# Optimization experiments

Hardware: AMD Instinct MI355X
Metric: run time of the kernel (lower is better)

The kernel has to match this reference:

```python
import jax, jax.numpy as jnp
import numpy as np

B, IN_CAPS, IN_DIM = 64, 2048, 16
NUM_CAPS, OUT_DIM = 32, 16
NUM_ROUTING = 3


def squash(v, axis=-1):
    # scale = |v|^2 / (1 + |v|^2) / |v|  (faithful to source, no epsilon)
    s2 = jnp.sum(jnp.square(v), axis=axis, keepdims=True)
    scale = s2 / (1.0 + s2) / jnp.sqrt(s2)
    return scale * v


def setup_inputs() -> dict:
    key = jax.random.key(0)
    k1, k2 = jax.random.split(key)
    inputs = jax.random.normal(k1, (B, IN_CAPS, IN_DIM), dtype=jnp.float32)
    # glorot-ish scaled transform matrices
    W = jax.random.normal(k2, (IN_CAPS, NUM_CAPS, IN_DIM, OUT_DIM), dtype=jnp.float32) * 0.05
    return {"inputs": inputs, "W": W}


def reference(inputs, W):
    # Prediction vectors u_hat[b,i,k,:] = inputs[b,i,:] @ W[i,k,:,:]
    u_hat = jnp.einsum('bid,ikdo->biko', inputs, W)  # [B, I, K, O]
    # Routing logits b (per-batch; source initializes from zeros and accumulates agreement)
    b = jnp.zeros(u_hat.shape[:3], dtype=u_hat.dtype)  # [B, I, K]
    v = None
    for i in range(NUM_ROUTING):
        c = jax.nn.softmax(b, axis=2)                      # coupling coeffs over output caps K
        s = jnp.einsum('bik,biko->bko', c, u_hat)          # weighted sum over input caps I
        v = squash(s)                                      # [B, K, O]
        if i != NUM_ROUTING - 1:
            b = b + jnp.einsum('biko,bko->bik', u_hat, v)  # agreement update
    return v  # [B, NUM_CAPS, OUT_DIM]
```

## Files before the change

### kernel.cpp

```cpp
#include <hip/hip_runtime.h>
#include <math.h>
#include <stdint.h>

#define NB 64
#define NI 2048
#define NK 32
#define ND 16

typedef _Float16 h2t   __attribute__((ext_vector_type(2)));
typedef _Float16 f16x4 __attribute__((ext_vector_type(4)));
typedef float    f32x4 __attribute__((ext_vector_type(4)));

#if defined(__has_builtin)
#if __has_builtin(__builtin_amdgcn_global_load_lds)
#define HAVE_GLL 1
#endif
#endif
#ifndef HAVE_GLL
#define HAVE_GLL 0
#endif

static __device__ __forceinline__ uint32_t pack_h2(float a, float b) {
    h2t p; p.x = (_Float16)a; p.y = (_Float16)b;
    return __builtin_bit_cast(uint32_t, p);
}

static __device__ __forceinline__ float swz_xor16(float x) {
    int v = __builtin_amdgcn_ds_swizzle(__builtin_bit_cast(int, x), 0x401F);
    return __builtin_bit_cast(float, v);
}
static __device__ __forceinline__ float xreduce_o(float p) {
    p += swz_xor16(p);
    p += __shfl_xor(p, 32);
    return p;
}

__global__ __launch_bounds__(256)
void conv_wx(const float* __restrict__ Wg, uint32_t* __restrict__ Wh,
             const float* __restrict__ X,  uint32_t* __restrict__ XT)
{
    __shared__ float tile[32 * 264];
    const int t = threadIdx.x;
    if (blockIdx.x < 2048) {
        const int i = blockIdx.x;
        const float4* src = (const float4*)(Wg + (size_t)i * 8192);
#pragma unroll
        for (int j = 0; j < 8; ++j) {
            const int f4 = t + j * 256;
            const int k  = f4 >> 6;
            const int r4 = f4 & 63;
            *(float4*)(&tile[k * 264 + r4 * 4]) = src[f4];
        }
        __syncthreads();
        const int T  = t >> 3;
        const int l0 = (t & 7) * 8;
        const float* s = tile + T * 264;
        uint2* dst = (uint2*)(Wh + (size_t)i * 4096) + T * 64 + l0;
#pragma unroll
        for (int n = 0; n < 8; ++n) {
            const int l = l0 + n;
            const int q = l >> 4, r = l & 15;
            uint2 u;
            u.x = pack_h2(s[(4 * q + 0) * 16 + r], s[(4 * q + 1) * 16 + r]);
            u.y = pack_h2(s[(4 * q + 2) * 16 + r], s[(4 * q + 3) * 16 + r]);
            dst[n] = u;
        }
    } else {
        const int g = (blockIdx.x - 2048) * 256 + t;
        const int b = g >> 11, i = g & 2047;
        const float4* src = (const float4*)(X + ((size_t)b * 2048 + i) * 16);
        const float4 f0 = src[0], f1 = src[1], f2 = src[2], f3 = src[3];
        uint4 o0, o1;
        o0.x = pack_h2(f0.x, f0.y); o0.y = pack_h2(f0.z, f0.w);
        o0.z = pack_h2(f1.x, f1.y); o0.w = pack_h2(f1.z, f1.w);
        o1.x = pack_h2(f2.x, f2.y); o1.y = pack_h2(f2.z, f2.w);
        o1.z = pack_h2(f3.x, f3.y); o1.w = pack_h2(f3.z, f3.w);
        uint4* dst = (uint4*)(XT + (size_t)i * 512 + b * 8);
        dst[0] = o0; dst[1] = o1;
    }
}

template<int VMODE>
__global__ __launch_bounds__(256, 3)
void caps_pass_m(const uint32_t* __restrict__ XT,
                 const uint32_t* __restrict__ Wh,
                 const float* __restrict__ V,
                 uint32_t* __restrict__ part_h)
{
    constexpr int IC = 16;
    __shared__ uint32_t Ws[2][4096];
    __shared__ uint32_t Xs[2048];
    __shared__ float    Ep[2][4][16];

    const int t = threadIdx.x;
    const int l = t & 63;
    const int w = t >> 6;
    const int r = l & 15;
    const int q = l >> 4;

    const int wg     = blockIdx.x;
    const int xcd    = wg & 7;
    const int slot   = wg >> 3;
    const int ichunk = xcd * 16 + (slot >> 2);
    const int bg     = slot & 3;
    const int i0 = ichunk * IC;
    const int b0 = bg * 16;

    f32x4 s_acc[8];
#pragma unroll
    for (int tt = 0; tt < 8; ++tt) s_acc[tt] = (f32x4){0.f, 0.f, 0.f, 0.f};

    f32x4 v_r[8];
    if constexpr (VMODE == 1) {
#pragma unroll
        for (int tt = 0; tt < 8; ++tt)
            v_r[tt] = *(const f32x4*)(V + ((size_t)(b0 + r) * NK + (8 * w + tt)) * 16 + 4 * q);
    }

    {
        const int ig = t >> 4, uu = t & 15;
        const uint4* src = (const uint4*)(XT + (size_t)(i0 + ig) * 512 + b0 * 8);
        *(uint4*)&Xs[ig * 128 + uu * 4]        = src[uu];
        *(uint4*)&Xs[ig * 128 + (uu + 16) * 4] = src[uu + 16];
    }

#if HAVE_GLL
#define STAGE_T(sl, tile)                                                      \
    {                                                                          \
        const size_t ibase_ = (size_t)(tile) * 4096;                           \
        _Pragma("unroll")                                                      \
        for (int jj = 0; jj < 4; ++jj) {                                       \
            const int p = w * 4 + jj;                                          \
            __builtin_amdgcn_global_load_lds(                                  \
                (const __attribute__((address_space(1))) void*)(Wh + ibase_ + p * 256 + l * 4), \
                (__attribute__((address_space(3))) void*)&Ws[sl][p * 256], 16, 0, 0); \
        }                                                                      \
    }
#define WAIT_V(n) { asm volatile("s_waitcnt vmcnt(" #n ")" ::: "memory");      \
                    __builtin_amdgcn_sched_barrier(0); }
#else
#define STAGE_T(sl, tile)                                                      \
    {                                                                          \
        const size_t ibase_ = (size_t)(tile) * 4096;                           \
        _Pragma("unroll")                                                      \
        for (int jj = 0; jj < 4; ++jj) {                                       \
            const int p = w * 4 + jj;                                          \
            ((uint4*)&Ws[sl][p * 256])[l] = *(const uint4*)(Wh + ibase_ + p * 256 + l * 4); \
        }                                                                      \
    }
#define WAIT_V(n) { asm volatile("s_waitcnt vmcnt(0) lgkmcnt(0)" ::: "memory");\
                    __builtin_amdgcn_sched_barrier(0); }
#endif
#define BAR_E() asm volatile("s_waitcnt lgkmcnt(0)\ns_barrier" ::: "memory");
#define STAGE_GUARD() { asm volatile("s_waitcnt lgkmcnt(0)" ::: "memory");     \
                        __builtin_amdgcn_sched_barrier(0); }

    __syncthreads();

    STAGE_T(0, i0)
    STAGE_T(1, i0 + 1)

    for (int ii = 0; ii < IC; ++ii) {
        const int cur = ii & 1;
        if (ii + 1 < IC) { WAIT_V(4) } else { WAIT_V(0) }

        const f16x4 xb = *(const f16x4*)&Xs[ii * 128 + r * 8 + q * 2];

        if constexpr (VMODE == 0) {
#pragma unroll
            for (int tt = 0; tt < 8; ++tt) {
                const f16x4 a = *(const f16x4*)&Ws[cur][(w * 8 + tt) * 128 + l * 2];
                s_acc[tt] = __builtin_amdgcn_mfma_f32_16x16x16f16(a, xb, s_acc[tt], 0, 0, 0);
            }
        } else {
            f32x4 um[8];
#pragma unroll
            for (int tt = 0; tt < 8; ++tt) {
                const f16x4 a = *(const f16x4*)&Ws[cur][(w * 8 + tt) * 128 + l * 2];
                um[tt] = __builtin_amdgcn_mfma_f32_16x16x16f16(
                    a, xb, (f32x4){0.f, 0.f, 0.f, 0.f}, 0, 0, 0);
            }
            float e[8];
            float esp = 0.f;
#pragma unroll
            for (int tt = 0; tt < 8; ++tt) {
                float p = um[tt][0] * v_r[tt][0];
                p = fmaf(um[tt][1], v_r[tt][1], p);
                p = fmaf(um[tt][2], v_r[tt][2], p);
                p = fmaf(um[tt][3], v_r[tt][3], p);
                p = xreduce_o(p);
                e[tt] = __expf(p);
                esp += e[tt];
            }
            if (q == 0) Ep[ii & 1][w][r] = esp;
            BAR_E();
            const float es = Ep[ii & 1][0][r] + Ep[ii & 1][1][r]
                           + Ep[ii & 1][2][r] + Ep[ii & 1][3][r];
            const float ci = __builtin_amdgcn_rcpf(es);
#pragma unroll
            for (int tt = 0; tt < 8; ++tt) {
                const float c = e[tt] * ci;
                s_acc[tt][0] = fmaf(c, um[tt][0], s_acc[tt][0]);
                s_acc[tt][1] = fmaf(c, um[tt][1], s_acc[tt][1]);
                s_acc[tt][2] = fmaf(c, um[tt][2], s_acc[tt][2]);
                s_acc[tt][3] = fmaf(c, um[tt][3], s_acc[tt][3]);
            }
        }

        if (ii + 2 < IC) {
            STAGE_GUARD();
            STAGE_T(cur, i0 + ii + 2)
        }
    }
#undef STAGE_T
#undef WAIT_V
#undef BAR_E
#undef STAGE_GUARD

    uint32_t* base = part_h + (size_t)(bg * 128 + ichunk) * 4096 + r * 256 + 2 * q;
#pragma unroll
    for (int tt = 0; tt < 8; ++tt) {
        uint2 st;
        st.x = pack_h2(s_acc[tt][0], s_acc[tt][1]);
        st.y = pack_h2(s_acc[tt][2], s_acc[tt][3]);
        *(uint2*)(base + (8 * w + tt) * 8) = st;
    }
}

template<int RMODE>
__global__ __launch_bounds__(256)
void caps_reduce(const uint32_t* __restrict__ part_h,
                 const float* __restrict__ S0red,
                 float* __restrict__ S0out,
                 float* __restrict__ Vout)
{
    __shared__ float2 red[4][64];
    const int t   = threadIdx.x;
    const int jl  = t & 63;
    const int qc  = t >> 6;
    const int jb  = blockIdx.x * 64;
    const int j   = jb + jl;
    const int b   = j >> 8;
    const int bg  = b >> 4;
    const int loc = (b & 15) * 256 + (j & 255);
    const uint32_t* p = part_h + ((size_t)(bg * 128 + qc * 32)) * 4096 + loc;
    float sx = 0.f, sy = 0.f;
#pragma unroll 8
    for (int ic = 0; ic < 32; ++ic) {
        h2t v = __builtin_bit_cast(h2t, p[(size_t)ic * 4096]);
        sx += (float)v.x; sy += (float)v.y;
    }
    red[qc][jl] = make_float2(sx, sy);
    __syncthreads();
    if (t < 64) {
        const int jj = jb + t;
        float2 a0 = red[0][t], a1 = red[1][t], a2 = red[2][t], a3 = red[3][t];
        const float tx = a0.x + a1.x + a2.x + a3.x;
        const float ty = a0.y + a1.y + a2.y + a3.y;
        if constexpr (RMODE == 0) {
            S0out[2 * jj]     = tx;
            S0out[2 * jj + 1] = ty;
            const float vx = tx * (1.0f / 32.0f), vy = ty * (1.0f / 32.0f);
            float sq = vx * vx + vy * vy;
#pragma unroll
            for (int mask = 4; mask >= 1; mask >>= 1) sq += __shfl_xor(sq, mask);
            const float sc = sqrtf(sq) / (1.0f + sq);
            Vout[2 * jj]     = vx * sc;
            Vout[2 * jj + 1] = vy * sc;
        } else if constexpr (RMODE == 1) {
            const float v0x = S0red[2 * jj] * (1.0f / 32.0f);
            const float v0y = S0red[2 * jj + 1] * (1.0f / 32.0f);
            float sq0 = v0x * v0x + v0y * v0y;
#pragma unroll
            for (int mask = 4; mask >= 1; mask >>= 1) sq0 += __shfl_xor(sq0, mask);
            const float sc0 = sqrtf(sq0) / (1.0f + sq0);
            float sq1 = tx * tx + ty * ty;
#pragma unroll
            for (int mask = 4; mask >= 1; mask >>= 1) sq1 += __shfl_xor(sq1, mask);
            const float sc1 = sqrtf(sq1) / (1.0f + sq1);
            Vout[2 * jj]     = fmaf(v0x, sc0, tx * sc1);
            Vout[2 * jj + 1] = fmaf(v0y, sc0, ty * sc1);
        } else {
            float sq = tx * tx + ty * ty;
#pragma unroll
            for (int mask = 4; mask >= 1; mask >>= 1) sq += __shfl_xor(sq, mask);
            const float sc = sqrtf(sq) / (1.0f + sq);
            Vout[2 * jj]     = tx * sc;
            Vout[2 * jj + 1] = ty * sc;
        }
    }
}

template<int VMODE>
__global__ __launch_bounds__(256, 4)
void caps_pass_f32(const float* __restrict__ X,
                   const float* __restrict__ Wg,
                   const float* __restrict__ S0,
                   const float* __restrict__ S1,
                   float* __restrict__ Sout)
{
    constexpr int IC = 8;
    __shared__ float Ws[8192];
    __shared__ float Xs[2048];

    const int t   = threadIdx.x;
    const int kk  = t & 31;
    const int oh  = (t >> 5) & 1;
    const int bq4 = t >> 6;

    const int wg     = blockIdx.x;
    const int xcd    = wg & 7;
    const int slot   = wg >> 3;
    const int ichunk = xcd * 32 + (slot >> 2);
    const int bg     = slot & 3;
    const int i0 = ichunk * IC;
    const int b0 = bg * 16;

    float s_acc[4][8];
#pragma unroll
    for (int bb = 0; bb < 4; ++bb)
#pragma unroll
        for (int o = 0; o < 8; ++o) s_acc[bb][o] = 0.f;

    float v_r[4][8];
    if constexpr (VMODE >= 1) {
#pragma unroll
        for (int bb = 0; bb < 4; ++bb) {
            const int b = b0 + bq4 * 4 + bb;
            const float* p0 = S0 + ((size_t)b * NK + kk) * 16 + oh * 8;
            float4 a = *(const float4*)(p0);
            float4 c = *(const float4*)(p0 + 4);
            float val0[8] = {a.x,a.y,a.z,a.w,c.x,c.y,c.z,c.w};
            float sq0 = 0.f;
#pragma unroll
            for (int o = 0; o < 8; ++o) { val0[o] *= (1.0f/32.0f); sq0 = fmaf(val0[o], val0[o], sq0); }
            sq0 += __shfl_xor(sq0, 32);
            const float sc0 = sqrtf(sq0) / (1.0f + sq0);
#pragma unroll
            for (int o = 0; o < 8; ++o) v_r[bb][o] = val0[o] * sc0;
            if constexpr (VMODE == 2) {
                const float* p1 = S1 + ((size_t)b * NK + kk) * 16 + oh * 8;
                float4 a1 = *(const float4*)(p1);
                float4 c1 = *(const float4*)(p1 + 4);
                float val1[8] = {a1.x,a1.y,a1.z,a1.w,c1.x,c1.y,c1.z,c1.w};
                float sq1 = 0.f;
#pragma unroll
                for (int o = 0; o < 8; ++o) sq1 = fmaf(val1[o], val1[o], sq1);
                sq1 += __shfl_xor(sq1, 32);
                const float sc1 = sqrtf(sq1) / (1.0f + sq1);
#pragma unroll
                for (int o = 0; o < 8; ++o) v_r[bb][o] = fmaf(val1[o], sc1, v_r[bb][o]);
            }
        }
    }

    {
        const int xb   = t >> 4;
        const int xig  = t & 7;
        const int half = (t >> 3) & 1;
        const float* xp = X + (size_t)(b0 + xb) * (NI * ND) + (size_t)(i0 + xig) * ND + half * 8;
        float4 f0 = *(const float4*)(xp);
        float4 f1 = *(const float4*)(xp + 4);
        float vals[8] = {f0.x,f0.y,f0.z,f0.w,f1.x,f1.y,f1.z,f1.w};
        const int m = (xig & 7) << 3;
#pragma unroll
        for (int jj = 0; jj < 8; ++jj) {
            const int d = half * 8 + jj;
            Xs[xig * 256 + ((16 * d + xb) ^ m)] = vals[jj];
        }
    }

    for (int ii = 0; ii < IC; ++ii) {
        const int i = i0 + ii;
        __syncthreads();
        {
            const float4* wsrc = (const float4*)(Wg + (size_t)i * 8192);
#pragma unroll
            for (int j = 0; j < 8; ++j) {
                float4 val = wsrc[t + j * 256];
                const int k = (t >> 6) + 4 * j;
                ((float4*)Ws)[k * 64 + ((t & 63) ^ (k & 7))] = val;
            }
        }
        __syncthreads();

        const int xm = (ii & 7) << 3;
        float u[4][8];
        if constexpr (VMODE >= 1) {
#pragma unroll
            for (int bb = 0; bb < 4; ++bb)
#pragma unroll
                for (int o = 0; o < 8; ++o) u[bb][o] = 0.f;
        }
#pragma unroll
        for (int d = 0; d < 16; ++d) {
            const float4 x4 = *(const float4*)(&Xs[ii * 256 + ((16 * d + 4 * bq4) ^ xm)]);
            float wvv[8];
            {
                const float4 wA = ((const float4*)Ws)[kk * 64 + ((d * 4 + oh * 2)     ^ (kk & 7))];
                const float4 wB = ((const float4*)Ws)[kk * 64 + ((d * 4 + oh * 2 + 1) ^ (kk & 7))];
                wvv[0]=wA.x; wvv[1]=wA.y; wvv[2]=wA.z; wvv[3]=wA.w;
                wvv[4]=wB.x; wvv[5]=wB.y; wvv[6]=wB.z; wvv[7]=wB.w;
            }
            if constexpr (VMODE >= 1) {
#pragma unroll
                for (int o = 0; o < 8; ++o) {
                    u[0][o] = fmaf(x4.x, wvv[o], u[0][o]);
                    u[1][o] = fmaf(x4.y, wvv[o], u[1][o]);
                    u[2][o] = fmaf(x4.z, wvv[o], u[2][o]);
                    u[3][o] = fmaf(x4.w, wvv[o], u[3][o]);
                }
            } else {
#pragma unroll
                for (int o = 0; o < 8; ++o) {
                    s_acc[0][o] = fmaf(x4.x, wvv[o], s_acc[0][o]);
                    s_acc[1][o] = fmaf(x4.y, wvv[o], s_acc[1][o]);
                    s_acc[2][o] = fmaf(x4.z, wvv[o], s_acc[2][o]);
                    s_acc[3][o] = fmaf(x4.w, wvv[o], s_acc[3][o]);
                }
            }
        }

        if constexpr (VMODE >= 1) {
#pragma unroll
            for (int bb = 0; bb < 4; ++bb) {
                float lg = 0.f;
#pragma unroll
                for (int o = 0; o < 8; ++o) lg = fmaf(u[bb][o], v_r[bb][o], lg);
                lg += __shfl_xor(lg, 32);
                float m = lg;
#pragma unroll
                for (int mask = 16; mask >= 1; mask >>= 1)
                    m = fmaxf(m, __shfl_xor(m, mask));
                const float e = __expf(lg - m);
                float ssum = e;
#pragma unroll
                for (int mask = 16; mask >= 1; mask >>= 1)
                    ssum += __shfl_xor(ssum, mask);
                const float c = e / ssum;
#pragma unroll
                for (int o = 0; o < 8; ++o)
                    s_acc[bb][o] = fmaf(c, u[bb][o], s_acc[bb][o]);
            }
        }
    }

#pragma unroll
    for (int bb = 0; bb < 4; ++bb) {
        float* sp = Sout + ((size_t)(b0 + bq4 * 4 + bb) * NK + kk) * 16 + oh * 8;
#pragma unroll
        for (int o = 0; o < 8; ++o) atomicAdd(sp + o, s_acc[bb][o]);
    }
}

__global__ __launch_bounds__(256)
void squash_kernel(const float* __restrict__ S, float* __restrict__ Vout)
{
    const int idx = blockIdx.x * 256 + threadIdx.x;
    float val = S[idx];
    float sq = val * val;
#pragma unroll
    for (int mask = 8; mask >= 1; mask >>= 1) sq += __shfl_xor(sq, mask);
    const float sc = sqrtf(sq) / (1.0f + sq);
    Vout[idx] = val * sc;
}

extern "C" void kernel_launch(void* const* d_in, const int* in_sizes, int n_in,
                              void* d_out, int out_size, void* d_ws, size_t ws_size,
                              hipStream_t stream)
{
    const float* X  = (const float*)d_in[0];
    const float* Wg = (const float*)d_in[1];
    float* out = (float*)d_out;

    const size_t WHU   = (size_t)2048 * 4096;
    const size_t XHU   = (size_t)64 * 2048 * 8;
    const size_t PARTU = (size_t)512 * 4096;
    const size_t need  = (WHU + XHU + PARTU) * 4 + 3 * 32768 * 4;

    const dim3 blk(256), pgrid(512), rgrid(256);

    if (ws_size >= need) {
        uint32_t* Wh   = (uint32_t*)d_ws;
        uint32_t* XT   = Wh + WHU;
        uint32_t* part = XT + XHU;
        float* s0      = (float*)(part + PARTU);
        float* v0      = s0 + 32768;
        float* v01     = v0 + 32768;

        conv_wx<<<dim3(2560), blk, 0, stream>>>(Wg, Wh, X, XT);

        caps_pass_m<0><<<pgrid, blk, 0, stream>>>(XT, Wh, nullptr, part);
        caps_reduce<0><<<rgrid, blk, 0, stream>>>(part, nullptr, s0, v0);
        caps_pass_m<1><<<pgrid, blk, 0, stream>>>(XT, Wh, v0, part);
        caps_reduce<1><<<rgrid, blk, 0, stream>>>(part, s0, nullptr, v01);
        caps_pass_m<1><<<pgrid, blk, 0, stream>>>(XT, Wh, v01, part);
        caps_reduce<2><<<rgrid, blk, 0, stream>>>(part, nullptr, nullptr, out);
    } else {
        float* s0 = (float*)d_ws;
        float* s1 = s0 + 32768;
        float* s2 = s1 + 32768;
        hipMemsetAsync(d_ws, 0, (size_t)3 * 32768 * sizeof(float), stream);
        caps_pass_f32<0><<<dim3(1024), blk, 0, stream>>>(X, Wg, nullptr, nullptr, s0);
        caps_pass_f32<1><<<dim3(1024), blk, 0, stream>>>(X, Wg, s0, nullptr, s1);
        caps_pass_f32<2><<<dim3(1024), blk, 0, stream>>>(X, Wg, s0, s1, s2);
        squash_kernel<<<dim3(128), blk, 0, stream>>>(s2, out);
    }
}
```

Before: 95.68 us.

## Widen capsule pass blocks to 32 batches with 512 threads to reuse W tiles

Each caps_pass_m block now covers 32 batch rows instead of 16 and uses 8 waves of 512 threads, with each wave doing 4 output capsules for two batch halves. Each staged W tile is reused across twice as many batches, so W traffic from global memory and the grid size are both halved. The partial-sum layout and the reduce kernel indexing are updated to match. In exchange there are fewer blocks (256) to fill the GPU, larger LDS per block, a softmax barrier per half, and a new launch bound of 512 threads that changes register limits.

Result: slower. 117.7 us (+23.0%).

```diff
diff --git a/kernel.cpp b/kernel.cpp
--- a/kernel.cpp
+++ b/kernel.cpp
@@ -81,7 +81,7 @@
 }
 
 template<int VMODE>
-__global__ __launch_bounds__(256, 3)
+__global__ __launch_bounds__(512, 4)
 void caps_pass_m(const uint32_t* __restrict__ XT,
                  const uint32_t* __restrict__ Wh,
                  const float* __restrict__ V,
@@ -89,8 +89,8 @@
 {
     constexpr int IC = 16;
     __shared__ uint32_t Ws[2][4096];
-    __shared__ uint32_t Xs[2048];
-    __shared__ float    Ep[2][4][16];
+    __shared__ uint32_t Xs[4096];
+    __shared__ float    Ep[2][2][8][16];
 
     const int t = threadIdx.x;
     const int l = t & 63;
@@ -101,52 +101,52 @@
     const int wg     = blockIdx.x;
     const int xcd    = wg & 7;
     const int slot   = wg >> 3;
-    const int ichunk = xcd * 16 + (slot >> 2);
-    const int bg     = slot & 3;
+    const int ichunk = xcd * 16 + (slot >> 1);
+    const int bg     = slot & 1;
     const int i0 = ichunk * IC;
-    const int b0 = bg * 16;
-
-    f32x4 s_acc[8];
-#pragma unroll
-    for (int tt = 0; tt < 8; ++tt) s_acc[tt] = (f32x4){0.f, 0.f, 0.f, 0.f};
-
-    f32x4 v_r[8];
+    const int b0 = bg * 32;
+
+    f32x4 s_acc[2][4];
+#pragma unroll
+    for (int h = 0; h < 2; ++h)
+#pragma unroll
+        for (int tt = 0; tt < 4; ++tt) s_acc[h][tt] = (f32x4){0.f, 0.f, 0.f, 0.f};
+
+    f32x4 v_r[2][4];
     if constexpr (VMODE == 1) {
 #pragma unroll
-        for (int tt = 0; tt < 8; ++tt)
-            v_r[tt] = *(const f32x4*)(V + ((size_t)(b0 + r) * NK + (8 * w + tt)) * 16 + 4 * q);
+        for (int h = 0; h < 2; ++h)
+#pragma unroll
+            for (int tt = 0; tt < 4; ++tt)
+                v_r[h][tt] = *(const f32x4*)(V + ((size_t)(b0 + h * 16 + r) * NK + (4 * w + tt)) * 16 + 4 * q);
     }
 
     {
-        const int ig = t >> 4, uu = t & 15;
-        const uint4* src = (const uint4*)(XT + (size_t)(i0 + ig) * 512 + b0 * 8);
-        *(uint4*)&Xs[ig * 128 + uu * 4]        = src[uu];
-        *(uint4*)&Xs[ig * 128 + (uu + 16) * 4] = src[uu + 16];
+        const int ig = t >> 5, b32 = t & 31;
+        const uint4* src = (const uint4*)(XT + (size_t)(i0 + ig) * 512 + b0 * 8 + b32 * 8);
+        *(uint4*)&Xs[ig * 256 + b32 * 8]     = src[0];
+        *(uint4*)&Xs[ig * 256 + b32 * 8 + 4] = src[1];
     }
 
 #if HAVE_GLL
 #define STAGE_T(sl, tile)                                                      \
     {                                                                          \
-        const size_t ibase_ = (size_t)(tile) * 4096;                           \
-        _Pragma("unroll")                                                      \
-        for (int jj = 0; jj < 4; ++jj) {                                       \
-            const int p = w * 4 + jj;                                          \
-            __builtin_amdgcn_global_load_lds(                                  \
-                (const __attribute__((address_space(1))) void*)(Wh + ibase_ + p * 256 + l * 4), \
-                (__attribute__((address_space(3))) void*)&Ws[sl][p * 256], 16, 0, 0); \
-        }                                                                      \
+        const size_t ibase_ = (size_t)(tile) * 4096 + w * 512;                 \
+        __builtin_amdgcn_global_load_lds(                                      \
+            (const __attribute__((address_space(1))) void*)(Wh + ibase_ + l * 4), \
+            (__attribute__((address_space(3))) void*)&Ws[sl][w * 512], 16, 0, 0); \
+        __builtin_amdgcn_global_load_lds(                                      \
+            (const __attribute__((address_space(1))) void*)(Wh + ibase_ + 256 + l * 4), \
+            (__attribute__((address_space(3))) void*)&Ws[sl][w * 512 + 256], 16, 0, 0); \
     }
 #define WAIT_V(n) { asm volatile("s_waitcnt vmcnt(" #n ")" ::: "memory");      \
                     __builtin_amdgcn_sched_barrier(0); }
 #else
 #define STAGE_T(sl, tile)                                                      \
     {                                                                          \
-        const size_t ibase_ = (size_t)(tile) * 4096;                           \
-        _Pragma("unroll")                                                      \
-        for (int jj = 0; jj < 4; ++jj) {                                       \
-            const int p = w * 4 + jj;                                          \
-            ((uint4*)&Ws[sl][p * 256])[l] = *(const uint4*)(Wh + ibase_ + p * 256 + l * 4); \
-        }                                                                      \
+        const size_t ibase_ = (size_t)(tile) * 4096 + w * 512;                 \
+        ((uint4*)&Ws[sl][w * 512])[l]       = *(const uint4*)(Wh + ibase_ + l * 4); \
+        ((uint4*)&Ws[sl][w * 512 + 256])[l] = *(const uint4*)(Wh + ibase_ + 256 + l * 4); \
     }
 #define WAIT_V(n) { asm volatile("s_waitcnt vmcnt(0) lgkmcnt(0)" ::: "memory");\
                     __builtin_amdgcn_sched_barrier(0); }
@@ -162,48 +162,55 @@
 
     for (int ii = 0; ii < IC; ++ii) {
         const int cur = ii & 1;
-        if (ii + 1 < IC) { WAIT_V(4) } else { WAIT_V(0) }
-
-        const f16x4 xb = *(const f16x4*)&Xs[ii * 128 + r * 8 + q * 2];
+        if (ii + 1 < IC) { WAIT_V(2) } else { WAIT_V(0) }
+
+        const f16x4 xb0 = *(const f16x4*)&Xs[ii * 256 + (0 * 16 + r) * 8 + q * 2];
+        const f16x4 xb1 = *(const f16x4*)&Xs[ii * 256 + (1 * 16 + r) * 8 + q * 2];
 
         if constexpr (VMODE == 0) {
 #pragma unroll
-            for (int tt = 0; tt < 8; ++tt) {
-                const f16x4 a = *(const f16x4*)&Ws[cur][(w * 8 + tt) * 128 + l * 2];
-                s_acc[tt] = __builtin_amdgcn_mfma_f32_16x16x16f16(a, xb, s_acc[tt], 0, 0, 0);
+            for (int tt = 0; tt < 4; ++tt) {
+                const f16x4 a = *(const f16x4*)&Ws[cur][(4 * w + tt) * 128 + l * 2];
+                s_acc[0][tt] = __builtin_amdgcn_mfma_f32_16x16x16f16(a, xb0, s_acc[0][tt], 0, 0, 0);
+                s_acc[1][tt] = __builtin_amdgcn_mfma_f32_16x16x16f16(a, xb1, s_acc[1][tt], 0, 0, 0);
             }
         } else {
-            f32x4 um[8];
-#pragma unroll
-            for (int tt = 0; tt < 8; ++tt) {
-                const f16x4 a = *(const f16x4*)&Ws[cur][(w * 8 + tt) * 128 + l * 2];
-                um[tt] = __builtin_amdgcn_mfma_f32_16x16x16f16(
-                    a, xb, (f32x4){0.f, 0.f, 0.f, 0.f}, 0, 0, 0);
-            }
-            float e[8];
-            float esp = 0.f;
-#pragma unroll
-            for (int tt = 0; tt < 8; ++tt) {
-                float p = um[tt][0] * v_r[tt][0];
-                p = fmaf(um[tt][1], v_r[tt][1], p);
-                p = fmaf(um[tt][2], v_r[tt][2], p);
-                p = fmaf(um[tt][3], v_r[tt][3], p);
-                p = xreduce_o(p);
-                e[tt] = __expf(p);
-                esp += e[tt];
-            }
-            if (q == 0) Ep[ii & 1][w][r] = esp;
-            BAR_E();
-            const float es = Ep[ii & 1][0][r] + Ep[ii & 1][1][r]
-                           + Ep[ii & 1][2][r] + Ep[ii & 1][3][r];
-            const float ci = __builtin_amdgcn_rcpf(es);
-#pragma unroll
-            for (int tt = 0; tt < 8; ++tt) {
-                const float c = e[tt] * ci;
-                s_acc[tt][0] = fmaf(c, um[tt][0], s_acc[tt][0]);
-                s_acc[tt][1] = fmaf(c, um[tt][1], s_acc[tt][1]);
-                s_acc[tt][2] = fmaf(c, um[tt][2], s_acc[tt][2]);
-                s_acc[tt][3] = fmaf(c, um[tt][3], s_acc[tt][3]);
+#pragma unroll
+            for (int h = 0; h < 2; ++h) {
+                const f16x4 xb = (h == 0) ? xb0 : xb1;
+                f32x4 um[4];
+#pragma unroll
+                for (int tt = 0; tt < 4; ++tt) {
+                    const f16x4 a = *(const f16x4*)&Ws[cur][(4 * w + tt) * 128 + l * 2];
+                    um[tt] = __builtin_amdgcn_mfma_f32_16x16x16f16(
+                        a, xb, (f32x4){0.f, 0.f, 0.f, 0.f}, 0, 0, 0);
+                }
+                float e[4];
+                float esp = 0.f;
+#pragma unroll
+                for (int tt = 0; tt < 4; ++tt) {
+                    float p = um[tt][0] * v_r[h][tt][0];
+                    p = fmaf(um[tt][1], v_r[h][tt][1], p);
+                    p = fmaf(um[tt][2], v_r[h][tt][2], p);
+                    p = fmaf(um[tt][3], v_r[h][tt][3], p);
+                    p = xreduce_o(p);
+                    e[tt] = __expf(p);
+                    esp += e[tt];
+                }
+                if (q == 0) Ep[ii & 1][h][w][r] = esp;
+                BAR_E();
+                float es = 0.f;
+#pragma unroll
+                for (int w2 = 0; w2 < 8; ++w2) es += Ep[ii & 1][h][w2][r];
+                const float ci = __builtin_amdgcn_rcpf(es);
+#pragma unroll
+                for (int tt = 0; tt < 4; ++tt) {
+                    const float c = e[tt] * ci;
+                    s_acc[h][tt][0] = fmaf(c, um[tt][0], s_acc[h][tt][0]);
+                    s_acc[h][tt][1] = fmaf(c, um[tt][1], s_acc[h][tt][1]);
+                    s_acc[h][tt][2] = fmaf(c, um[tt][2], s_acc[h][tt][2]);
+                    s_acc[h][tt][3] = fmaf(c, um[tt][3], s_acc[h][tt][3]);
+                }
             }
         }
 
@@ -217,14 +224,16 @@
 #undef BAR_E
 #undef STAGE_GUARD
 
-    uint32_t* base = part_h + (size_t)(bg * 128 + ichunk) * 4096 + r * 256 + 2 * q;
-#pragma unroll
-    for (int tt = 0; tt < 8; ++tt) {
-        uint2 st;
-        st.x = pack_h2(s_acc[tt][0], s_acc[tt][1]);
-        st.y = pack_h2(s_acc[tt][2], s_acc[tt][3]);
-        *(uint2*)(base + (8 * w + tt) * 8) = st;
-    }
+    uint32_t* base = part_h + (size_t)(bg * 128 + ichunk) * 8192 + 2 * q;
+#pragma unroll
+    for (int h = 0; h < 2; ++h)
+#pragma unroll
+        for (int tt = 0; tt < 4; ++tt) {
+            uint2 st;
+            st.x = pack_h2(s_acc[h][tt][0], s_acc[h][tt][1]);
+            st.y = pack_h2(s_acc[h][tt][2], s_acc[h][tt][3]);
+            *(uint2*)(base + (h * 16 + r) * 256 + (4 * w + tt) * 8) = st;
+        }
 }
 
 template<int RMODE>
@@ -241,13 +250,13 @@
     const int jb  = blockIdx.x * 64;
     const int j   = jb + jl;
     const int b   = j >> 8;
-    const int bg  = b >> 4;
-    const int loc = (b & 15) * 256 + (j & 255);
-    const uint32_t* p = part_h + ((size_t)(bg * 128 + qc * 32)) * 4096 + loc;
+    const int bg  = b >> 5;
+    const int loc = (b & 31) * 256 + (j & 255);
+    const uint32_t* p = part_h + ((size_t)(bg * 128 + qc * 32)) * 8192 + loc;
     float sx = 0.f, sy = 0.f;
 #pragma unroll 8
     for (int ic = 0; ic < 32; ++ic) {
-        h2t v = __builtin_bit_cast(h2t, p[(size_t)ic * 4096]);
+        h2t v = __builtin_bit_cast(h2t, p[(size_t)ic * 8192]);
         sx += (float)v.x; sy += (float)v.y;
     }
     red[qc][jl] = make_float2(sx, sy);
@@ -475,10 +484,10 @@
 
     const size_t WHU   = (size_t)2048 * 4096;
     const size_t XHU   = (size_t)64 * 2048 * 8;
-    const size_t PARTU = (size_t)512 * 4096;
+    const size_t PARTU = (size_t)256 * 8192;
     const size_t need  = (WHU + XHU + PARTU) * 4 + 3 * 32768 * 4;
 
-    const dim3 blk(256), pgrid(512), rgrid(256);
+    const dim3 blk(256), pblk(512), pgrid(256), rgrid(256);
 
     if (ws_size >= need) {
         uint32_t* Wh   = (uint32_t*)d_ws;
@@ -490,11 +499,11 @@
 
         conv_wx<<<dim3(2560), blk, 0, stream>>>(Wg, Wh, X, XT);
 
-        caps_pass_m<0><<<pgrid, blk, 0, stream>>>(XT, Wh, nullptr, part);
+        caps_pass_m<0><<<pgrid, pblk, 0, stream>>>(XT, Wh, nullptr, part);
         caps_reduce<0><<<rgrid, blk, 0, stream>>>(part, nullptr, s0, v0);
-        caps_pass_m<1><<<pgrid, blk, 0, stream>>>(XT, Wh, v0, part);
+        caps_pass_m<1><<<pgrid, pblk, 0, stream>>>(XT, Wh, v0, part);
         caps_reduce<1><<<rgrid, blk, 0, stream>>>(part, s0, nullptr, v01);
-        caps_pass_m<1><<<pgrid, blk, 0, stream>>>(XT, Wh, v01, part);
+        caps_pass_m<1><<<pgrid, pblk, 0, stream>>>(XT, Wh, v01, part);
         caps_reduce<2><<<rgrid, blk, 0, stream>>>(part, nullptr, nullptr, out);
     } else {
         float* s0 = (float*)d_ws;
```
